# Optimization experiments

Hardware: AMD Instinct MI355X
Metric: run time of the kernel (lower is better)

## Reference

```python
import jax, jax.numpy as jnp
import numpy as np

TEMP = 1.0
EPS = 1e-15

B, N, F, K = 8, 2000, 128, 64


def setup_inputs() -> dict:
    key = jax.random.key(0)
    k1, k2, k3 = jax.random.split(key, 3)
    x = jax.random.normal(k1, (B, N, F), dtype=jnp.float32)
    adj = jax.random.uniform(k2, (B, N, N), dtype=jnp.float32)
    s = jax.random.normal(k3, (B, N, K), dtype=jnp.float32)
    mask = jnp.ones((B, N), dtype=bool)
    return {"x": x, "adj": adj, "s": s, "mask": mask}


def reference(x, adj, s, mask):
    k = s.shape[-1]
    s = jax.nn.softmax(s / TEMP, axis=-1)
    m = mask[..., None].astype(x.dtype)          # [B,N,1]
    x = x * m
    s = s * m

    # pooled features: s^T x -> [B,K,F]
    out = jnp.einsum('bnk,bnf->bkf', s, x)

    # pooled adjacency: s^T A s -> [B,K,K]
    as_ = jnp.einsum('bnm,bmk->bnk', adj, s)     # A s, [B,N,K]
    out_adj = jnp.einsum('bnk,bnl->bkl', as_, s)

    # mincut loss
    mincut_num = jnp.einsum('bkk->b', out_adj)
    d_flat = jnp.sum(adj, axis=-1)               # degree, [B,N]
    # trace(s^T diag(d) s) = sum_n d_n * sum_k s_nk^2 (avoids dense diag)
    mincut_den = jnp.einsum('bn,bnk,bnk->b', d_flat, s, s)
    mincut_loss = jnp.mean(-(mincut_num / mincut_den))

    # orthogonality loss
    ss = jnp.einsum('bnk,bnl->bkl', s, s)        # [B,K,K]
    ss_norm = jnp.linalg.norm(ss, axis=(-2, -1), keepdims=True)
    i_s = jnp.eye(k, dtype=ss.dtype)
    ortho = jnp.linalg.norm(ss / ss_norm - i_s / jnp.sqrt(jnp.asarray(k, ss.dtype)), axis=(-2, -1))
    ortho_loss = jnp.mean(ortho)

    # zero diagonal, symmetric degree normalization
    ind = jnp.arange(k)
    out_adj = out_adj.at[:, ind, ind].set(0.0)
    d = jnp.sqrt(jnp.sum(out_adj, axis=-1))[:, None, :] + EPS  # [B,1,K]
    out_adj = out_adj / d / jnp.swapaxes(d, 1, 2)

    return out, out_adj, mincut_loss, ortho_loss
```

## Files before the change

### kernel.cpp

```cpp
#include <hip/hip_runtime.h>

typedef __bf16 bf16;
typedef __bf16 bf16x4 __attribute__((ext_vector_type(4)));
typedef __bf16 bf16x8 __attribute__((ext_vector_type(8)));
typedef float f32x4 __attribute__((ext_vector_type(4)));

#define NB 8
#define NN 2000
#define N2 2048
#define KK 64
#define FF 128

__global__ __launch_bounds__(256) void k1_softmax(const float* __restrict__ s,
                                                  bf16* __restrict__ sT,
                                                  float* __restrict__ rowsq) {
  const int b = blockIdx.x >> 5, tile = blockIdx.x & 31;
  const int n0 = tile * 64;
  const int t = threadIdx.x;
  const int r = t >> 2, q = t & 3;
  __shared__ float ptile[64][65];
  const int n = n0 + r;
  const bool valid = n < NN;
  float v[16];
  if (valid) {
    const float4* src = (const float4*)(s + ((size_t)(b * NN + n)) * KK + q * 16);
#pragma unroll
    for (int i = 0; i < 4; ++i) {
      float4 f = src[i];
      v[4 * i + 0] = f.x; v[4 * i + 1] = f.y; v[4 * i + 2] = f.z; v[4 * i + 3] = f.w;
    }
  } else {
#pragma unroll
    for (int i = 0; i < 16; ++i) v[i] = 0.f;
  }
  float mx = v[0];
#pragma unroll
  for (int i = 1; i < 16; ++i) mx = fmaxf(mx, v[i]);
  mx = fmaxf(mx, __shfl_xor(mx, 1));
  mx = fmaxf(mx, __shfl_xor(mx, 2));
  float sum = 0.f;
#pragma unroll
  for (int i = 0; i < 16; ++i) { v[i] = __expf(v[i] - mx); sum += v[i]; }
  sum += __shfl_xor(sum, 1);
  sum += __shfl_xor(sum, 2);
  const float scale = valid ? (1.0f / sum) : 0.f;
  float rq = 0.f;
#pragma unroll
  for (int i = 0; i < 16; ++i) { v[i] *= scale; rq += v[i] * v[i]; }
  rq += __shfl_xor(rq, 1);
  rq += __shfl_xor(rq, 2);
  if (q == 0) rowsq[b * N2 + n0 + r] = rq;
#pragma unroll
  for (int i = 0; i < 16; ++i) ptile[r][q * 16 + i] = v[i];
  __syncthreads();
  bf16x8 o0, o1;
#pragma unroll
  for (int i = 0; i < 8; ++i) o0[i] = (bf16)ptile[q * 16 + i][r];
#pragma unroll
  for (int i = 0; i < 8; ++i) o1[i] = (bf16)ptile[q * 16 + 8 + i][r];
  bf16* dst = sT + ((size_t)(b * KK + r)) * N2 + n0 + q * 16;
  *(bf16x8*)dst = o0;
  *(bf16x8*)(dst + 8) = o1;
}

__global__ __launch_bounds__(256) void k1b_xt(const float* __restrict__ x,
                                              bf16* __restrict__ xT) {
  const int b = blockIdx.x >> 5, tile = blockIdx.x & 31;
  const int n0 = tile * 64;
  const int t = threadIdx.x;
  __shared__ float xt[64 * 132];
#pragma unroll
  for (int i = 0; i < 8; ++i) {
    int idx = t + 256 * i;
    int row = idx >> 5, c4 = idx & 31;
    int n = n0 + row;
    float4 vv = make_float4(0.f, 0.f, 0.f, 0.f);
    if (n < NN) vv = ((const float4*)(x + ((size_t)(b * NN + n)) * FF))[c4];
    *(float4*)&xt[row * 132 + c4 * 4] = vv;
  }
  __syncthreads();
  const int f = t >> 1, h = t & 1;
  bf16* dst = xT + ((size_t)(b * FF + f)) * N2 + n0 + h * 32;
#pragma unroll
  for (int g = 0; g < 4; ++g) {
    bf16x8 o;
#pragma unroll
    for (int i = 0; i < 8; ++i) o[i] = (bf16)xt[(h * 32 + g * 8 + i) * 132 + f];
    *(bf16x8*)(dst + g * 8) = o;
  }
}

__global__ __launch_bounds__(256) void k2_adjs(const float* __restrict__ adj,
                                               const bf16* __restrict__ sT,
                                               bf16* __restrict__ asT,
                                               const float* __restrict__ rowsq,
                                               float* __restrict__ den_part) {
  const int b = blockIdx.x >> 7, tile = blockIdx.x & 127;
  const int n0 = tile * 16;
  const int t = threadIdx.x;
  if (n0 >= NN) {
    if (t == 0) den_part[b * 128 + tile] = 0.f;
    const int k = t >> 2, nseg = t & 3;
    bf16x4 z = {(bf16)0.f, (bf16)0.f, (bf16)0.f, (bf16)0.f};
    *(bf16x4*)(asT + ((size_t)(b * KK + k)) * N2 + n0 + nseg * 4) = z;
    return;
  }
  const int w = t >> 6, l = t & 63;
  const int lr = l & 15, lg = l >> 4;
  const float* arow = adj + ((size_t)(b * NN + n0 + lr)) * NN;
  const bf16* sbase = sT + (size_t)b * KK * N2;
  f32x4 acc[4];
#pragma unroll
  for (int ct = 0; ct < 4; ++ct)
#pragma unroll
    for (int r = 0; r < 4; ++r) acc[ct][r] = 0.f;
  const int m_begin = w * 512;
#pragma unroll 4
  for (int s = 0; s < 16; ++s) {
    const int m0 = m_begin + s * 32;
    int ma = m0 + lg * 8;
    if (ma > NN - 8) ma = NN - 8;
    const float4 a0 = *(const float4*)(arow + ma);
    const float4 a1 = *(const float4*)(arow + ma + 4);
    bf16x8 af;
    af[0] = (bf16)a0.x; af[1] = (bf16)a0.y; af[2] = (bf16)a0.z; af[3] = (bf16)a0.w;
    af[4] = (bf16)a1.x; af[5] = (bf16)a1.y; af[6] = (bf16)a1.z; af[7] = (bf16)a1.w;
    const int mb = m0 + lg * 8;
#pragma unroll
    for (int ct = 0; ct < 4; ++ct) {
      bf16x8 bfv = *(const bf16x8*)(sbase + (size_t)(ct * 16 + lr) * N2 + mb);
      acc[ct] = __builtin_amdgcn_mfma_f32_16x16x32_bf16(af, bfv, acc[ct], 0, 0, 0);
    }
  }
  __shared__ float red[4][16][64];
  __shared__ float outv[16][64];
  __shared__ float dnsh[16];
#pragma unroll
  for (int ct = 0; ct < 4; ++ct)
#pragma unroll
    for (int r = 0; r < 4; ++r)
      red[w][lg * 4 + r][ct * 16 + lr] = acc[ct][r];
  __syncthreads();
  const int n = t >> 4, k4 = t & 15;
  float dsum = 0.f;
#pragma unroll
  for (int j = 0; j < 4; ++j) {
    const int kk = k4 * 4 + j;
    const float v = red[0][n][kk] + red[1][n][kk] + red[2][n][kk] + red[3][n][kk];
    outv[n][kk] = v;
    dsum += v;
  }
  dsum += __shfl_xor(dsum, 1);
  dsum += __shfl_xor(dsum, 2);
  dsum += __shfl_xor(dsum, 4);
  dsum += __shfl_xor(dsum, 8);
  if (k4 == 0) dnsh[n] = dsum * rowsq[b * N2 + n0 + n];
  __syncthreads();
  if (t == 0) {
    float dtot = 0.f;
#pragma unroll
    for (int i = 0; i < 16; ++i) dtot += dnsh[i];
    den_part[b * 128 + tile] = dtot;
  }
  const int k = t >> 2, nseg = t & 3;
  bf16x4 o;
#pragma unroll
  for (int j = 0; j < 4; ++j) o[j] = (bf16)outv[nseg * 4 + j][k];
  *(bf16x4*)(asT + ((size_t)(b * KK + k)) * N2 + n0 + nseg * 4) = o;
}

__global__ __launch_bounds__(256) void k3_gemms(const bf16* __restrict__ sT,
                                                const bf16* __restrict__ asT,
                                                const bf16* __restrict__ xT,
                                                float* __restrict__ adjraw,
                                                float* __restrict__ ssw,
                                                float* __restrict__ dout) {
  const int b = blockIdx.x >> 6, u = blockIdx.x & 63;
  const bf16 *Ab, *Bb;
  float* Cb;
  int ldC;
  if (u < 16) {
    const int rt = u >> 2, ct = u & 3;
    Ab = asT + ((size_t)(b * KK + rt * 16)) * N2;
    Bb = sT + ((size_t)(b * KK + ct * 16)) * N2;
    Cb = adjraw + b * KK * KK + rt * 16 * KK + ct * 16; ldC = KK;
  } else if (u < 32) {
    const int v = u - 16, rt = v >> 2, ct = v & 3;
    Ab = sT + ((size_t)(b * KK + rt * 16)) * N2;
    Bb = sT + ((size_t)(b * KK + ct * 16)) * N2;
    Cb = ssw + b * KK * KK + rt * 16 * KK + ct * 16; ldC = KK;
  } else {
    const int v = u - 32, rt = v >> 3, ct = v & 7;
    Ab = sT + ((size_t)(b * KK + rt * 16)) * N2;
    Bb = xT + ((size_t)(b * FF + ct * 16)) * N2;
    Cb = dout + b * KK * FF + rt * 16 * FF + ct * 16; ldC = FF;
  }
  const int t = threadIdx.x;
  const int w = t >> 6, l = t & 63;
  const int lr = l & 15, lg = l >> 4;
  f32x4 acc;
#pragma unroll
  for (int r = 0; r < 4; ++r) acc[r] = 0.f;
  const int m_begin = w * 512;
#pragma unroll 4
  for (int s = 0; s < 16; ++s) {
    const int m = m_begin + s * 32 + lg * 8;
    bf16x8 af = *(const bf16x8*)(Ab + (size_t)lr * N2 + m);
    bf16x8 bfv = *(const bf16x8*)(Bb + (size_t)lr * N2 + m);
    acc = __builtin_amdgcn_mfma_f32_16x16x32_bf16(af, bfv, acc, 0, 0, 0);
  }
  __shared__ float red[4][16][16];
#pragma unroll
  for (int r = 0; r < 4; ++r) red[w][lg * 4 + r][lr] = acc[r];
  __syncthreads();
  const int row = t >> 4, col = t & 15;
  const float v = red[0][row][col] + red[1][row][col] +
                  red[2][row][col] + red[3][row][col];
  Cb[row * ldC + col] = v;
}

__device__ inline float wred64(float v) {
#pragma unroll
  for (int off = 32; off > 0; off >>= 1) v += __shfl_xor(v, off);
  return v;
}

__global__ __launch_bounds__(64) void k4_final(const float* __restrict__ adjraw,
                                               const float* __restrict__ ssw,
                                               const float* __restrict__ den_part,
                                               float* __restrict__ dout,
                                               float* __restrict__ loss_part) {
  const int b = blockIdx.x;
  const int lane = threadIdx.x;
  const float dp = den_part[b * 128 + lane] + den_part[b * 128 + 64 + lane];
  const float den = wred64(dp);
  const float* arow = adjraw + b * 4096 + lane * 64;
  float4 av[16];
#pragma unroll
  for (int i = 0; i < 16; ++i) av[i] = ((const float4*)arow)[i];
  const float diag = adjraw[b * 4096 + lane * 65];
  float rs = 0.f;
#pragma unroll
  for (int i = 0; i < 16; ++i) rs += av[i].x + av[i].y + av[i].z + av[i].w;
  rs -= diag;
  rs = fmaxf(rs, 0.f);
  const float num = wred64(diag);
  const float d = sqrtf(rs) + 1e-15f;
  __shared__ float dsh[64];
  dsh[lane] = d;
  __syncthreads();
  const float invd = 1.0f / d;
  float* orow = dout + NB * KK * FF + b * 4096 + lane * 64;
#pragma unroll
  for (int i = 0; i < 16; ++i) {
    float4 cvv = av[i];
    cvv.x = (4 * i + 0 == lane) ? 0.f : cvv.x * invd / dsh[4 * i + 0];
    cvv.y = (4 * i + 1 == lane) ? 0.f : cvv.y * invd / dsh[4 * i + 1];
    cvv.z = (4 * i + 2 == lane) ? 0.f : cvv.z * invd / dsh[4 * i + 2];
    cvv.w = (4 * i + 3 == lane) ? 0.f : cvv.w * invd / dsh[4 * i + 3];
    ((float4*)orow)[i] = cvv;
  }
  const float* srow = ssw + b * 4096 + lane * 64;
  float4 sv[16];
  float sq = 0.f;
#pragma unroll
  for (int i = 0; i < 16; ++i) {
    sv[i] = ((const float4*)srow)[i];
    sq += sv[i].x * sv[i].x + sv[i].y * sv[i].y + sv[i].z * sv[i].z + sv[i].w * sv[i].w;
  }
  const float frob = sqrtf(wred64(sq));
  const float fi = 1.0f / frob;
  float osum = 0.f;
#pragma unroll
  for (int i = 0; i < 16; ++i) {
    float tx = sv[i].x * fi - ((4 * i + 0 == lane) ? 0.125f : 0.f);
    float ty = sv[i].y * fi - ((4 * i + 1 == lane) ? 0.125f : 0.f);
    float tz = sv[i].z * fi - ((4 * i + 2 == lane) ? 0.125f : 0.f);
    float tw = sv[i].w * fi - ((4 * i + 3 == lane) ? 0.125f : 0.f);
    osum += tx * tx + ty * ty + tz * tz + tw * tw;
  }
  const float ot = wred64(osum);
  if (lane == 0) {
    loss_part[b] = -(num / den);
    loss_part[8 + b] = sqrtf(ot);
  }
}

__global__ void k5_loss(const float* __restrict__ loss_part, float* __restrict__ dout) {
  if (threadIdx.x == 0 && blockIdx.x == 0) {
    float m = 0.f, o = 0.f;
    for (int b2 = 0; b2 < 8; ++b2) { m += loss_part[b2]; o += loss_part[8 + b2]; }
    dout[NB * KK * FF + NB * KK * KK + 0] = m * 0.125f;
    dout[NB * KK * FF + NB * KK * KK + 1] = o * 0.125f;
  }
}

extern "C" void kernel_launch(void* const* d_in, const int* in_sizes, int n_in,
                              void* d_out, int out_size, void* d_ws, size_t ws_size,
                              hipStream_t stream) {
  const float* x = (const float*)d_in[0];
  const float* adj = (const float*)d_in[1];
  const float* s = (const float*)d_in[2];
  float* out = (float*)d_out;
  char* ws = (char*)d_ws;
  bf16* sT = (bf16*)ws;
  bf16* xT = (bf16*)(ws + (2u << 20));
  bf16* asT = (bf16*)(ws + (6u << 20));
  float* rowsq = (float*)(ws + (8u << 20));
  float* den_part = (float*)(ws + (8u << 20) + 65536);
  float* adjraw = (float*)(ws + (8u << 20) + 65536 + 4096);
  float* ssw = adjraw + NB * KK * KK;
  float* loss_part = ssw + NB * KK * KK;

  k1_softmax<<<256, 256, 0, stream>>>(s, sT, rowsq);
  k1b_xt<<<256, 256, 0, stream>>>(x, xT);
  k2_adjs<<<1024, 256, 0, stream>>>(adj, sT, asT, rowsq, den_part);
  k3_gemms<<<512, 256, 0, stream>>>(sT, asT, xT, adjraw, ssw, out);
  k4_final<<<8, 64, 0, stream>>>(adjraw, ssw, den_part, out, loss_part);
  k5_loss<<<1, 64, 0, stream>>>(loss_part, out);
}
```

Before: 248.7 us.

## Fuse x transpose into adjacency GEMM kernel and merge final loss kernels

Folds the x-transpose kernel into the A·s kernel as extra blocks and merges the loss-reduction kernel into a single-block final kernel, cutting two launches. The A·s kernel is restructured: each block stages 16 adjacency rows per 128-column chunk into a double-buffered, XOR-swizzled LDS tile as bf16, and each of its four waves computes one 16-column slice of K over the full row, replacing the cross-wave LDS reduction. This adds a barrier per chunk and serialises the whole adjacency stream within a block, trading memory-level parallelism for less reduction work and fewer launches.

```diff
diff --git a/kernel.cpp b/kernel.cpp
--- a/kernel.cpp
+++ b/kernel.cpp
@@ -63,110 +63,124 @@
   *(bf16x8*)(dst + 8) = o1;
 }
 
-__global__ __launch_bounds__(256) void k1b_xt(const float* __restrict__ x,
-                                              bf16* __restrict__ xT) {
-  const int b = blockIdx.x >> 5, tile = blockIdx.x & 31;
-  const int n0 = tile * 64;
+__device__ __forceinline__ bf16x8 cvt8(float4 a, float4 b) {
+  bf16x8 v;
+  v[0] = (bf16)a.x; v[1] = (bf16)a.y; v[2] = (bf16)a.z; v[3] = (bf16)a.w;
+  v[4] = (bf16)b.x; v[5] = (bf16)b.y; v[6] = (bf16)b.z; v[7] = (bf16)b.w;
+  return v;
+}
+
+__global__ __launch_bounds__(256) void k2_fused(const float* __restrict__ adj,
+                                                const bf16* __restrict__ sT,
+                                                const float* __restrict__ x,
+                                                bf16* __restrict__ xT,
+                                                bf16* __restrict__ asT,
+                                                const float* __restrict__ rowsq,
+                                                float* __restrict__ den_part) {
+  __shared__ __align__(16) char smem[64 * 132 * 4];
+  const int bid = blockIdx.x;
   const int t = threadIdx.x;
-  __shared__ float xt[64 * 132];
-#pragma unroll
-  for (int i = 0; i < 8; ++i) {
-    int idx = t + 256 * i;
-    int row = idx >> 5, c4 = idx & 31;
-    int n = n0 + row;
-    float4 vv = make_float4(0.f, 0.f, 0.f, 0.f);
-    if (n < NN) vv = ((const float4*)(x + ((size_t)(b * NN + n)) * FF))[c4];
-    *(float4*)&xt[row * 132 + c4 * 4] = vv;
-  }
-  __syncthreads();
-  const int f = t >> 1, h = t & 1;
-  bf16* dst = xT + ((size_t)(b * FF + f)) * N2 + n0 + h * 32;
-#pragma unroll
-  for (int g = 0; g < 4; ++g) {
-    bf16x8 o;
-#pragma unroll
-    for (int i = 0; i < 8; ++i) o[i] = (bf16)xt[(h * 32 + g * 8 + i) * 132 + f];
-    *(bf16x8*)(dst + g * 8) = o;
-  }
-}
-
-__global__ __launch_bounds__(256) void k2_adjs(const float* __restrict__ adj,
-                                               const bf16* __restrict__ sT,
-                                               bf16* __restrict__ asT,
-                                               const float* __restrict__ rowsq,
-                                               float* __restrict__ den_part) {
-  const int b = blockIdx.x >> 7, tile = blockIdx.x & 127;
-  const int n0 = tile * 16;
-  const int t = threadIdx.x;
-  if (n0 >= NN) {
-    if (t == 0) den_part[b * 128 + tile] = 0.f;
-    const int k = t >> 2, nseg = t & 3;
-    bf16x4 z = {(bf16)0.f, (bf16)0.f, (bf16)0.f, (bf16)0.f};
-    *(bf16x4*)(asT + ((size_t)(b * KK + k)) * N2 + n0 + nseg * 4) = z;
+
+  if (bid >= 1024) {
+    float* xt = (float*)smem;
+    const int bb = (bid - 1024) >> 5, tl = (bid - 1024) & 31;
+    const int n0b = tl * 64;
+#pragma unroll
+    for (int i = 0; i < 8; ++i) {
+      int idx = t + 256 * i;
+      int row = idx >> 5, c4 = idx & 31;
+      int n = n0b + row;
+      float4 vv = make_float4(0.f, 0.f, 0.f, 0.f);
+      if (n < NN) vv = ((const float4*)(x + ((size_t)(bb * NN + n)) * FF))[c4];
+      *(float4*)&xt[row * 132 + c4 * 4] = vv;
+    }
+    __syncthreads();
+    const int f = t >> 1, h = t & 1;
+    bf16* dst = xT + ((size_t)(bb * FF + f)) * N2 + n0b + h * 32;
+#pragma unroll
+    for (int g = 0; g < 4; ++g) {
+      bf16x8 o;
+#pragma unroll
+      for (int i = 0; i < 8; ++i) o[i] = (bf16)xt[(h * 32 + g * 8 + i) * 132 + f];
+      *(bf16x8*)(dst + g * 8) = o;
+    }
     return;
   }
+
+  const int b = bid >> 7, tile = bid & 127;
+  if (tile >= 125) {
+    if (tile == 125) {
+      const int k = t >> 2, seg = t & 3;
+      bf16x4 z = {(bf16)0.f, (bf16)0.f, (bf16)0.f, (bf16)0.f};
+      bf16* p = asT + ((size_t)(b * KK + k)) * N2 + 2000 + seg * 12;
+      *(bf16x4*)(p + 0) = z; *(bf16x4*)(p + 4) = z; *(bf16x4*)(p + 8) = z;
+      if (t < 3) den_part[b * 128 + 125 + t] = 0.f;
+    }
+    return;
+  }
+
   const int w = t >> 6, l = t & 63;
   const int lr = l & 15, lg = l >> 4;
-  const float* arow = adj + ((size_t)(b * NN + n0 + lr)) * NN;
-  const bf16* sbase = sT + (size_t)b * KK * N2;
-  f32x4 acc[4];
-#pragma unroll
-  for (int ct = 0; ct < 4; ++ct)
-#pragma unroll
-    for (int r = 0; r < 4; ++r) acc[ct][r] = 0.f;
-  const int m_begin = w * 512;
-#pragma unroll 4
-  for (int s = 0; s < 16; ++s) {
-    const int m0 = m_begin + s * 32;
-    int ma = m0 + lg * 8;
-    if (ma > NN - 8) ma = NN - 8;
-    const float4 a0 = *(const float4*)(arow + ma);
-    const float4 a1 = *(const float4*)(arow + ma + 4);
-    bf16x8 af;
-    af[0] = (bf16)a0.x; af[1] = (bf16)a0.y; af[2] = (bf16)a0.z; af[3] = (bf16)a0.w;
-    af[4] = (bf16)a1.x; af[5] = (bf16)a1.y; af[6] = (bf16)a1.z; af[7] = (bf16)a1.w;
-    const int mb = m0 + lg * 8;
-#pragma unroll
-    for (int ct = 0; ct < 4; ++ct) {
-      bf16x8 bfv = *(const bf16x8*)(sbase + (size_t)(ct * 16 + lr) * N2 + mb);
-      acc[ct] = __builtin_amdgcn_mfma_f32_16x16x32_bf16(af, bfv, acc[ct], 0, 0, 0);
-    }
-  }
-  __shared__ float red[4][16][64];
-  __shared__ float outv[16][64];
-  __shared__ float dnsh[16];
-#pragma unroll
-  for (int ct = 0; ct < 4; ++ct)
-#pragma unroll
-    for (int r = 0; r < 4; ++r)
-      red[w][lg * 4 + r][ct * 16 + lr] = acc[ct][r];
-  __syncthreads();
-  const int n = t >> 4, k4 = t & 15;
-  float dsum = 0.f;
-#pragma unroll
-  for (int j = 0; j < 4; ++j) {
-    const int kk = k4 * 4 + j;
-    const float v = red[0][n][kk] + red[1][n][kk] + red[2][n][kk] + red[3][n][kk];
-    outv[n][kk] = v;
-    dsum += v;
-  }
-  dsum += __shfl_xor(dsum, 1);
-  dsum += __shfl_xor(dsum, 2);
-  dsum += __shfl_xor(dsum, 4);
-  dsum += __shfl_xor(dsum, 8);
-  if (k4 == 0) dnsh[n] = dsum * rowsq[b * N2 + n0 + n];
-  __syncthreads();
-  if (t == 0) {
-    float dtot = 0.f;
-#pragma unroll
-    for (int i = 0; i < 16; ++i) dtot += dnsh[i];
-    den_part[b * 128 + tile] = dtot;
-  }
-  const int k = t >> 2, nseg = t & 3;
+  const int n0 = tile * 16;
+  bf16* abuf = (bf16*)smem;
+  float* dred = (float*)(smem + 8192);
+
+  const int srow = t >> 4, scol = t & 15;
+  const float* rowb = adj + ((size_t)(b * NN + n0 + srow)) * NN;
+  bf16* wp = abuf + srow * 128 + ((scol ^ (srow & 7)) * 8);
+  const bf16* sTw = sT + ((size_t)(b * KK + w * 16 + lr)) * N2;
+  const bf16* arp = abuf + lr * 128;
+
+  f32x4 acc;
+#pragma unroll
+  for (int r = 0; r < 4; ++r) acc[r] = 0.f;
+
+  {
+    const int mc = scol * 8;
+    float4 A0 = *(const float4*)(rowb + mc);
+    float4 A1 = *(const float4*)(rowb + mc + 4);
+    *(bf16x8*)wp = cvt8(A0, A1);
+  }
+
+  for (int c = 0; c < 16; ++c) {
+    __syncthreads();
+    float4 A0, A1;
+    if (c < 15) {
+      int m1 = (c + 1) * 128 + scol * 8;
+      int mc = m1 > 1992 ? 1992 : m1;
+      A0 = *(const float4*)(rowb + mc);
+      A1 = *(const float4*)(rowb + mc + 4);
+    }
+    const bf16* sTc = sTw + c * 128;
+    const bf16* ac = arp + (c & 1) * 2048;
+#pragma unroll
+    for (int st = 0; st < 4; ++st) {
+      bf16x8 bfrag = *(const bf16x8*)(sTc + st * 32 + lg * 8);
+      bf16x8 afrag = *(const bf16x8*)(ac + (((st * 4 + lg) ^ (lr & 7)) * 8));
+      acc = __builtin_amdgcn_mfma_f32_16x16x32_bf16(afrag, bfrag, acc, 0, 0, 0);
+    }
+    if (c < 15)
+      *(bf16x8*)(wp + ((c + 1) & 1) * 2048) = cvt8(A0, A1);
+  }
+
   bf16x4 o;
 #pragma unroll
-  for (int j = 0; j < 4; ++j) o[j] = (bf16)outv[nseg * 4 + j][k];
-  *(bf16x4*)(asT + ((size_t)(b * KK + k)) * N2 + n0 + nseg * 4) = o;
+  for (int r = 0; r < 4; ++r) o[r] = (bf16)acc[r];
+  *(bf16x4*)(asT + ((size_t)(b * KK + w * 16 + lr)) * N2 + n0 + lg * 4) = o;
+
+  float s0 = acc[0], s1 = acc[1], s2 = acc[2], s3 = acc[3];
+#pragma unroll
+  for (int off = 1; off <= 8; off <<= 1) {
+    s0 += __shfl_xor(s0, off); s1 += __shfl_xor(s1, off);
+    s2 += __shfl_xor(s2, off); s3 += __shfl_xor(s3, off);
+  }
+  const float* rqp = rowsq + b * N2 + n0 + lg * 4;
+  float part = s0 * rqp[0] + s1 * rqp[1] + s2 * rqp[2] + s3 * rqp[3];
+  part += __shfl_xor(part, 16);
+  part += __shfl_xor(part, 32);
+  if (l == 0) dred[w] = part;
+  __syncthreads();
+  if (t == 0) den_part[b * 128 + tile] = dred[0] + dred[1] + dred[2] + dred[3];
 }
 
 __global__ __launch_bounds__(256) void k3_gemms(const bf16* __restrict__ sT,
@@ -225,13 +239,12 @@
   return v;
 }
 
-__global__ __launch_bounds__(64) void k4_final(const float* __restrict__ adjraw,
-                                               const float* __restrict__ ssw,
-                                               const float* __restrict__ den_part,
-                                               float* __restrict__ dout,
-                                               float* __restrict__ loss_part) {
-  const int b = blockIdx.x;
-  const int lane = threadIdx.x;
+__global__ __launch_bounds__(512) void k4_final(const float* __restrict__ adjraw,
+                                                const float* __restrict__ ssw,
+                                                const float* __restrict__ den_part,
+                                                float* __restrict__ dout) {
+  const int b = threadIdx.x >> 6;
+  const int lane = threadIdx.x & 63;
   const float dp = den_part[b * 128 + lane] + den_part[b * 128 + 64 + lane];
   const float den = wred64(dp);
   const float* arow = adjraw + b * 4096 + lane * 64;
@@ -246,18 +259,19 @@
   rs = fmaxf(rs, 0.f);
   const float num = wred64(diag);
   const float d = sqrtf(rs) + 1e-15f;
-  __shared__ float dsh[64];
-  dsh[lane] = d;
+  __shared__ float dsh[8][64];
+  __shared__ float lossm[8], losso[8];
+  dsh[b][lane] = d;
   __syncthreads();
   const float invd = 1.0f / d;
   float* orow = dout + NB * KK * FF + b * 4096 + lane * 64;
 #pragma unroll
   for (int i = 0; i < 16; ++i) {
     float4 cvv = av[i];
-    cvv.x = (4 * i + 0 == lane) ? 0.f : cvv.x * invd / dsh[4 * i + 0];
-    cvv.y = (4 * i + 1 == lane) ? 0.f : cvv.y * invd / dsh[4 * i + 1];
-    cvv.z = (4 * i + 2 == lane) ? 0.f : cvv.z * invd / dsh[4 * i + 2];
-    cvv.w = (4 * i + 3 == lane) ? 0.f : cvv.w * invd / dsh[4 * i + 3];
+    cvv.x = (4 * i + 0 == lane) ? 0.f : cvv.x * invd / dsh[b][4 * i + 0];
+    cvv.y = (4 * i + 1 == lane) ? 0.f : cvv.y * invd / dsh[b][4 * i + 1];
+    cvv.z = (4 * i + 2 == lane) ? 0.f : cvv.z * invd / dsh[b][4 * i + 2];
+    cvv.w = (4 * i + 3 == lane) ? 0.f : cvv.w * invd / dsh[b][4 * i + 3];
     ((float4*)orow)[i] = cvv;
   }
   const float* srow = ssw + b * 4096 + lane * 64;
@@ -281,17 +295,16 @@
   }
   const float ot = wred64(osum);
   if (lane == 0) {
-    loss_part[b] = -(num / den);
-    loss_part[8 + b] = sqrtf(ot);
-  }
-}
-
-__global__ void k5_loss(const float* __restrict__ loss_part, float* __restrict__ dout) {
-  if (threadIdx.x == 0 && blockIdx.x == 0) {
-    float m = 0.f, o = 0.f;
-    for (int b2 = 0; b2 < 8; ++b2) { m += loss_part[b2]; o += loss_part[8 + b2]; }
+    lossm[b] = -(num / den);
+    losso[b] = sqrtf(ot);
+  }
+  __syncthreads();
+  if (threadIdx.x == 0) {
+    float m = 0.f, oo = 0.f;
+#pragma unroll
+    for (int b2 = 0; b2 < 8; ++b2) { m += lossm[b2]; oo += losso[b2]; }
     dout[NB * KK * FF + NB * KK * KK + 0] = m * 0.125f;
-    dout[NB * KK * FF + NB * KK * KK + 1] = o * 0.125f;
+    dout[NB * KK * FF + NB * KK * KK + 1] = oo * 0.125f;
   }
 }
 
@@ -310,12 +323,9 @@
   float* den_part = (float*)(ws + (8u << 20) + 65536);
   float* adjraw = (float*)(ws + (8u << 20) + 65536 + 4096);
   float* ssw = adjraw + NB * KK * KK;
-  float* loss_part = ssw + NB * KK * KK;
 
   k1_softmax<<<256, 256, 0, stream>>>(s, sT, rowsq);
-  k1b_xt<<<256, 256, 0, stream>>>(x, xT);
-  k2_adjs<<<1024, 256, 0, stream>>>(adj, sT, asT, rowsq, den_part);
+  k2_fused<<<1280, 256, 0, stream>>>(adj, sT, x, xT, asT, rowsq, den_part);
   k3_gemms<<<512, 256, 0, stream>>>(sT, asT, xT, adjraw, ssw, out);
-  k4_final<<<8, 64, 0, stream>>>(adjraw, ssw, den_part, out, loss_part);
-  k5_loss<<<1, 64, 0, stream>>>(loss_part, out);
-}
+  k4_final<<<1, 512, 0, stream>>>(adjraw, ssw, den_part, out);
+}
```

Result: faster. 235.0 us (-5.5%).

## Fuse x transpose into adjacency GEMM and stage adj rows through swizzled LDS

Applied to the files above, without the earlier changes.

The x-transpose kernel now runs as extra blocks of the adjacency GEMM launch, which saves one launch and lets both pieces of work run together. The A·s loop now has each wave load contiguous 128-column chunks of adj with coalesced float4 reads. It converts them to bf16 into a double-buffered, XOR-swizzled LDS tile and overlaps the next chunk's global loads with the current chunk's MFMAs. Padding tiles beyond N are now skipped and only the tail columns of asT are zeroed. k4 therefore ignores the den_part entries that are no longer written.

```diff
diff --git a/kernel.cpp b/kernel.cpp
--- a/kernel.cpp
+++ b/kernel.cpp
@@ -63,91 +63,147 @@
   *(bf16x8*)(dst + 8) = o1;
 }
 
-__global__ __launch_bounds__(256) void k1b_xt(const float* __restrict__ x,
-                                              bf16* __restrict__ xT) {
-  const int b = blockIdx.x >> 5, tile = blockIdx.x & 31;
-  const int n0 = tile * 64;
+__global__ __launch_bounds__(256) void k2_fused(const float* __restrict__ adj,
+                                                const bf16* __restrict__ sT,
+                                                const float* __restrict__ x,
+                                                bf16* __restrict__ xT,
+                                                bf16* __restrict__ asT,
+                                                const float* __restrict__ rowsq,
+                                                float* __restrict__ den_part) {
+  __shared__ __align__(16) char smem[33792];
+  const int bid = blockIdx.x;
   const int t = threadIdx.x;
-  __shared__ float xt[64 * 132];
-#pragma unroll
-  for (int i = 0; i < 8; ++i) {
-    int idx = t + 256 * i;
-    int row = idx >> 5, c4 = idx & 31;
-    int n = n0 + row;
-    float4 vv = make_float4(0.f, 0.f, 0.f, 0.f);
-    if (n < NN) vv = ((const float4*)(x + ((size_t)(b * NN + n)) * FF))[c4];
-    *(float4*)&xt[row * 132 + c4 * 4] = vv;
-  }
-  __syncthreads();
-  const int f = t >> 1, h = t & 1;
-  bf16* dst = xT + ((size_t)(b * FF + f)) * N2 + n0 + h * 32;
-#pragma unroll
-  for (int g = 0; g < 4; ++g) {
-    bf16x8 o;
-#pragma unroll
-    for (int i = 0; i < 8; ++i) o[i] = (bf16)xt[(h * 32 + g * 8 + i) * 132 + f];
-    *(bf16x8*)(dst + g * 8) = o;
-  }
-}
-
-__global__ __launch_bounds__(256) void k2_adjs(const float* __restrict__ adj,
-                                               const bf16* __restrict__ sT,
-                                               bf16* __restrict__ asT,
-                                               const float* __restrict__ rowsq,
-                                               float* __restrict__ den_part) {
-  const int b = blockIdx.x >> 7, tile = blockIdx.x & 127;
+
+  if (bid >= 1024) {
+    float* xt = (float*)smem;
+    const int bb = (bid - 1024) >> 5, tl = (bid - 1024) & 31;
+    const int n0b = tl * 64;
+#pragma unroll
+    for (int i = 0; i < 8; ++i) {
+      int idx = t + 256 * i;
+      int row = idx >> 5, c4 = idx & 31;
+      int n = n0b + row;
+      float4 vv = make_float4(0.f, 0.f, 0.f, 0.f);
+      if (n < NN) vv = ((const float4*)(x + ((size_t)(bb * NN + n)) * FF))[c4];
+      *(float4*)&xt[row * 132 + c4 * 4] = vv;
+    }
+    __syncthreads();
+    const int f = t >> 1, h = t & 1;
+    bf16* dst = xT + ((size_t)(bb * FF + f)) * N2 + n0b + h * 32;
+#pragma unroll
+    for (int g = 0; g < 4; ++g) {
+      bf16x8 o;
+#pragma unroll
+      for (int i = 0; i < 8; ++i) o[i] = (bf16)xt[(h * 32 + g * 8 + i) * 132 + f];
+      *(bf16x8*)(dst + g * 8) = o;
+    }
+    return;
+  }
+
+  const int b = bid >> 7, tile = bid & 127;
+  if (tile >= 125) {
+    if (tile == 125) {
+      const int k = t >> 2, seg = t & 3;
+      bf16x4 z = {(bf16)0.f, (bf16)0.f, (bf16)0.f, (bf16)0.f};
+      bf16* p = asT + ((size_t)(b * KK + k)) * N2 + 2000 + seg * 12;
+      *(bf16x4*)(p + 0) = z; *(bf16x4*)(p + 4) = z; *(bf16x4*)(p + 8) = z;
+    }
+    return;
+  }
+
+  const int w = t >> 6, l = t & 63;
   const int n0 = tile * 16;
-  const int t = threadIdx.x;
-  if (n0 >= NN) {
-    if (t == 0) den_part[b * 128 + tile] = 0.f;
-    const int k = t >> 2, nseg = t & 3;
-    bf16x4 z = {(bf16)0.f, (bf16)0.f, (bf16)0.f, (bf16)0.f};
-    *(bf16x4*)(asT + ((size_t)(b * KK + k)) * N2 + n0 + nseg * 4) = z;
-    return;
-  }
-  const int w = t >> 6, l = t & 63;
+  bf16* abuf = (bf16*)smem + w * 4096;
+
+  const int sr = l >> 2, cf = l & 3;
+  const float4* rowp = (const float4*)(adj + ((size_t)(b * NN + n0 + sr)) * NN);
+  const int srx = sr & 7;
+
   const int lr = l & 15, lg = l >> 4;
-  const float* arow = adj + ((size_t)(b * NN + n0 + lr)) * NN;
-  const bf16* sbase = sT + (size_t)b * KK * N2;
+  const int lrx = lr & 7;
+  const bf16* sTb = sT + (size_t)b * KK * N2;
+
   f32x4 acc[4];
 #pragma unroll
-  for (int ct = 0; ct < 4; ++ct)
-#pragma unroll
-    for (int r = 0; r < 4; ++r) acc[ct][r] = 0.f;
-  const int m_begin = w * 512;
-#pragma unroll 4
-  for (int s = 0; s < 16; ++s) {
-    const int m0 = m_begin + s * 32;
-    int ma = m0 + lg * 8;
-    if (ma > NN - 8) ma = NN - 8;
-    const float4 a0 = *(const float4*)(arow + ma);
-    const float4 a1 = *(const float4*)(arow + ma + 4);
-    bf16x8 af;
-    af[0] = (bf16)a0.x; af[1] = (bf16)a0.y; af[2] = (bf16)a0.z; af[3] = (bf16)a0.w;
-    af[4] = (bf16)a1.x; af[5] = (bf16)a1.y; af[6] = (bf16)a1.z; af[7] = (bf16)a1.w;
-    const int mb = m0 + lg * 8;
-#pragma unroll
-    for (int ct = 0; ct < 4; ++ct) {
-      bf16x8 bfv = *(const bf16x8*)(sbase + (size_t)(ct * 16 + lr) * N2 + mb);
-      acc[ct] = __builtin_amdgcn_mfma_f32_16x16x32_bf16(af, bfv, acc[ct], 0, 0, 0);
-    }
-  }
-  __shared__ float red[4][16][64];
-  __shared__ float outv[16][64];
-  __shared__ float dnsh[16];
-#pragma unroll
-  for (int ct = 0; ct < 4; ++ct)
+  for (int kt = 0; kt < 4; ++kt)
+#pragma unroll
+    for (int r = 0; r < 4; ++r) acc[kt][r] = 0.f;
+
+  float4 L[8];
+
+#define K2_ISSUE(GC)                                                        \
+  {                                                                         \
+    const int fbase_ = (GC) * 32 + cf;                                      \
+    _Pragma("unroll")                                                       \
+    for (int j = 0; j < 8; ++j) {                                           \
+      int fi_ = fbase_ + 4 * j;                                             \
+      if ((GC) == 15 && fi_ > 499) fi_ = 499;   \
+      L[j] = rowp[fi_];                                                     \
+    }                                                                       \
+  }
+
+#define K2_WRITE(BUF)                                                       \
+  {                                                                         \
+    bf16* base_ = abuf + (BUF) * 2048 + sr * 128;                           \
+    _Pragma("unroll")                                                       \
+    for (int j = 0; j < 8; ++j) {                                           \
+      const int s8_ = cf + 4 * j;                                           \
+      bf16x4 v_;                                                            \
+      v_[0] = (bf16)L[j].x; v_[1] = (bf16)L[j].y;                           \
+      v_[2] = (bf16)L[j].z; v_[3] = (bf16)L[j].w;                           \
+      *(bf16x4*)(base_ + (((s8_ >> 1) ^ srx) << 3) + ((s8_ & 1) << 2)) = v_;\
+    }                                                                       \
+  }
+
+#define K2_MFMA(BUF, GC)                                                    \
+  {                                                                         \
+    const bf16* ab_ = abuf + (BUF) * 2048 + lr * 128;                       \
+    const int m0_ = (GC) * 128;                                             \
+    _Pragma("unroll")                                                       \
+    for (int st = 0; st < 4; ++st) {                                        \
+      bf16x8 af_ = *(const bf16x8*)(ab_ + ((((st << 2) + lg) ^ lrx) << 3)); \
+      _Pragma("unroll")                                                     \
+      for (int kt = 0; kt < 4; ++kt) {                                      \
+        bf16x8 bf_ = *(const bf16x8*)(sTb + (size_t)(kt * 16 + lr) * N2 +   \
+                                      m0_ + st * 32 + lg * 8);              \
+        acc[kt] = __builtin_amdgcn_mfma_f32_16x16x32_bf16(af_, bf_,         \
+                                                          acc[kt], 0, 0, 0);\
+      }                                                                     \
+    }                                                                       \
+  }
+
+  const int gc0 = w * 4;
+  K2_ISSUE(gc0);
+  K2_WRITE(0);
+  K2_ISSUE(gc0 + 1);
+#pragma unroll
+  for (int c = 0; c < 4; ++c) {
+    K2_MFMA(c & 1, gc0 + c);
+    if (c < 3) K2_WRITE((c + 1) & 1);
+    if (c < 2) K2_ISSUE(gc0 + c + 2);
+  }
+#undef K2_ISSUE
+#undef K2_WRITE
+#undef K2_MFMA
+
+  __syncthreads();
+  float* red = (float*)smem;
+  float* outv = (float*)(smem + 16384);
+  float* dnsh = (float*)(smem + 16384 + 4096);
+#pragma unroll
+  for (int kt = 0; kt < 4; ++kt)
 #pragma unroll
     for (int r = 0; r < 4; ++r)
-      red[w][lg * 4 + r][ct * 16 + lr] = acc[ct][r];
+      red[(w * 16 + lg * 4 + r) * 64 + kt * 16 + lr] = acc[kt][r];
   __syncthreads();
   const int n = t >> 4, k4 = t & 15;
   float dsum = 0.f;
 #pragma unroll
   for (int j = 0; j < 4; ++j) {
     const int kk = k4 * 4 + j;
-    const float v = red[0][n][kk] + red[1][n][kk] + red[2][n][kk] + red[3][n][kk];
-    outv[n][kk] = v;
+    const float v = red[(0 * 16 + n) * 64 + kk] + red[(1 * 16 + n) * 64 + kk] +
+                    red[(2 * 16 + n) * 64 + kk] + red[(3 * 16 + n) * 64 + kk];
+    outv[n * 64 + kk] = v;
     dsum += v;
   }
   dsum += __shfl_xor(dsum, 1);
@@ -165,7 +221,7 @@
   const int k = t >> 2, nseg = t & 3;
   bf16x4 o;
 #pragma unroll
-  for (int j = 0; j < 4; ++j) o[j] = (bf16)outv[nseg * 4 + j][k];
+  for (int j = 0; j < 4; ++j) o[j] = (bf16)outv[(nseg * 4 + j) * 64 + k];
   *(bf16x4*)(asT + ((size_t)(b * KK + k)) * N2 + n0 + nseg * 4) = o;
 }
 
@@ -232,7 +288,8 @@
                                                float* __restrict__ loss_part) {
   const int b = blockIdx.x;
   const int lane = threadIdx.x;
-  const float dp = den_part[b * 128 + lane] + den_part[b * 128 + 64 + lane];
+  const float dp = den_part[b * 128 + lane] +
+                   ((lane < 61) ? den_part[b * 128 + 64 + lane] : 0.f);
   const float den = wred64(dp);
   const float* arow = adjraw + b * 4096 + lane * 64;
   float4 av[16];
@@ -313,8 +370,7 @@
   float* loss_part = ssw + NB * KK * KK;
 
   k1_softmax<<<256, 256, 0, stream>>>(s, sT, rowsq);
-  k1b_xt<<<256, 256, 0, stream>>>(x, xT);
-  k2_adjs<<<1024, 256, 0, stream>>>(adj, sT, asT, rowsq, den_part);
+  k2_fused<<<1280, 256, 0, stream>>>(adj, sT, x, xT, asT, rowsq, den_part);
   k3_gemms<<<512, 256, 0, stream>>>(sT, asT, xT, adjraw, ssw, out);
   k4_final<<<8, 64, 0, stream>>>(adjraw, ssw, den_part, out, loss_part);
   k5_loss<<<1, 64, 0, stream>>>(loss_part, out);
```

Result: faster. 243.4 us (-2.1%).
